# Kernel tuning notes

Measured on AMD Instinct MI355X. Metric: run time of the kernel, lower is better.

## Reference

```python
import jax, jax.numpy as jnp
import numpy as np

N = 50000   # nodes
E = 800000  # edges (before self loops)
D = 128     # n_embd
H = 4       # heads
C = D // H  # per-head channels
NEG_SLOPE = 0.2
EPS = 1e-5


def _ln(x, w):
    m = jnp.mean(x, axis=-1, keepdims=True)
    v = jnp.mean((x - m) ** 2, axis=-1, keepdims=True)
    return (x - m) / jnp.sqrt(v + EPS) * w


def setup_inputs() -> dict:
    key = jax.random.key(0)
    ks = jax.random.split(key, 8)
    s = 0.02
    return {
        "x": jax.random.normal(ks[0], (N, D), jnp.float32),
        "edge_index": jax.random.randint(ks[1], (2, E), 0, N, jnp.int32),
        "ln1_w": jnp.ones((D,), jnp.float32),
        "Wl": jax.random.normal(ks[2], (D, D), jnp.float32) * s,
        "bl": jnp.zeros((D,), jnp.float32),
        "Wr": jax.random.normal(ks[3], (D, D), jnp.float32) * s,
        "br": jnp.zeros((D,), jnp.float32),
        "att": jax.random.normal(ks[4], (H, C), jnp.float32) * s,
        "gat_bias": jnp.zeros((D,), jnp.float32),
        "ln2_w": jnp.ones((D,), jnp.float32),
        "W_fc": jax.random.normal(ks[5], (D, 4 * D), jnp.float32) * s,
        "W_proj": jax.random.normal(ks[6], (4 * D, D), jnp.float32) * s,
    }


def reference(x, edge_index, ln1_w, Wl, bl, Wr, br, att, gat_bias, ln2_w, W_fc, W_proj):
    n = x.shape[0]
    # add self loops (GATv2Conv default)
    loops = jnp.arange(n, dtype=edge_index.dtype)
    src = jnp.concatenate([edge_index[0], loops])  # message sources (x_j)
    dst = jnp.concatenate([edge_index[1], loops])  # message targets (x_i)

    h = _ln(x, ln1_w)
    xl = (h @ Wl + bl).reshape(n, H, C)  # source transform
    xr = (h @ Wr + br).reshape(n, H, C)  # target transform

    # GATv2 edge-wise attention
    e = jax.nn.leaky_relu(xl[src] + xr[dst], NEG_SLOPE)      # [E+N, H, C]
    score = jnp.einsum('ehc,hc->eh', e, att)                  # [E+N, H]
    smax = jax.ops.segment_max(score, dst, num_segments=n)    # [N, H]
    ex = jnp.exp(score - smax[dst])
    denom = jax.ops.segment_sum(ex, dst, num_segments=n)      # [N, H]
    alpha = ex / denom[dst]                                   # segment softmax
    agg = jax.ops.segment_sum(alpha[:, :, None] * xl[src], dst, num_segments=n)

    x = x + agg.reshape(n, H * C) + gat_bias

    h2 = _ln(x, ln2_w)
    x = x + jax.nn.gelu(h2 @ W_fc, approximate=False) @ W_proj
    return x
```

## Files before the change

### kernel.cpp

```cpp
#include <hip/hip_runtime.h>
#include <math.h>

typedef __attribute__((ext_vector_type(8))) short bf16x8;
typedef __attribute__((ext_vector_type(4))) float f32x4;

__device__ __forceinline__ unsigned bf16b(float f) {
  unsigned u = __float_as_uint(f);
  return (u + 0x7fffu + ((u >> 16) & 1u)) >> 16;
}
__device__ __forceinline__ unsigned packbf(float lo, float hi) {
  return bf16b(lo) | (bf16b(hi) << 16);
}
__device__ __forceinline__ float unpk_lo(unsigned u) { return __uint_as_float(u << 16); }
__device__ __forceinline__ float unpk_hi(unsigned u) { return __uint_as_float(u & 0xffff0000u); }
__device__ __forceinline__ float gelu_f(float v) {
  return 0.5f * v * (1.0f + erff(v * 0.70710678118654752f));
}

__global__ void k_cvt(const float* __restrict__ src, unsigned short* __restrict__ dst,
                      int lgK, int C, int total) {
  int i = blockIdx.x * 256 + threadIdx.x;
  if (i < total) {
    int k = i & ((1 << lgK) - 1);
    int c = i >> lgK;
    dst[i] = (unsigned short)bf16b(src[(size_t)k * C + c]);
  }
}

__global__ __launch_bounds__(256, 2) void k_gemlr(
    const float* __restrict__ x, const float* __restrict__ ln1w,
    const unsigned short* __restrict__ Wl_t, const float* __restrict__ bl,
    const unsigned short* __restrict__ Wr_t, const float* __restrict__ br,
    unsigned short* __restrict__ xl16, unsigned short* __restrict__ xr16, int n)
{
  __shared__ __align__(16) unsigned short hs[64 * 128];
  const int t = threadIdx.x;
  const int lane = t & 63, w = t >> 6;
  const int r0 = blockIdx.x * 64;

  {
    const int row = t >> 2, seg = t & 3;
    const int gr = r0 + row;
    const float4* xr4 = (const float4*)(x + (size_t)(gr < n ? gr : 0) * 128) + seg * 8;
    float4 v[8];
    #pragma unroll
    for (int j = 0; j < 8; ++j) v[j] = (gr < n) ? xr4[j] : make_float4(0.f,0.f,0.f,0.f);
    float s = 0.f;
    #pragma unroll
    for (int j = 0; j < 8; ++j) s += v[j].x + v[j].y + v[j].z + v[j].w;
    s += __shfl_xor(s, 1); s += __shfl_xor(s, 2);
    const float mean = s * (1.0f / 128.0f);
    float vv = 0.f;
    #pragma unroll
    for (int j = 0; j < 8; ++j) {
      float a = v[j].x - mean, b = v[j].y - mean, c = v[j].z - mean, d = v[j].w - mean;
      vv += a * a + b * b + c * c + d * d;
    }
    vv += __shfl_xor(vv, 1); vv += __shfl_xor(vv, 2);
    const float rstd = rsqrtf(vv * (1.0f / 128.0f) + 1e-5f);
    #pragma unroll
    for (int j2 = 0; j2 < 4; ++j2) {
      float4 wa = ((const float4*)ln1w)[seg * 8 + 2 * j2];
      float4 wb = ((const float4*)ln1w)[seg * 8 + 2 * j2 + 1];
      const float4 va = v[2 * j2], vb = v[2 * j2 + 1];
      uint4 pk;
      pk.x = packbf((va.x - mean) * rstd * wa.x, (va.y - mean) * rstd * wa.y);
      pk.y = packbf((va.z - mean) * rstd * wa.z, (va.w - mean) * rstd * wa.w);
      pk.z = packbf((vb.x - mean) * rstd * wb.x, (vb.y - mean) * rstd * wb.y);
      pk.w = packbf((vb.z - mean) * rstd * wb.z, (vb.w - mean) * rstd * wb.w);
      int byteoff = (row * 256 + (seg * 4 + j2) * 16) ^ ((row & 7) << 4);
      *(uint4*)((char*)hs + byteoff) = pk;
    }
  }
  __syncthreads();

  const int l15 = lane & 15, lg = lane >> 4;
  const unsigned short* __restrict__ Wt = (w < 2) ? Wl_t : Wr_t;
  const float* __restrict__ bias = (w < 2) ? bl : br;
  unsigned short* __restrict__ outp = (w < 2) ? xl16 : xr16;
  const int cbase = (w & 1) * 64;

  f32x4 acc[4][4];
  #pragma unroll
  for (int m = 0; m < 4; ++m)
    #pragma unroll
    for (int nf = 0; nf < 4; ++nf) acc[m][nf] = (f32x4){0.f, 0.f, 0.f, 0.f};

  #pragma unroll
  for (int ks = 0; ks < 4; ++ks) {
    bf16x8 b[4];
    #pragma unroll
    for (int nf = 0; nf < 4; ++nf) {
      const int c = cbase + nf * 16 + l15;
      b[nf] = *(const bf16x8*)(Wt + (size_t)c * 128 + ks * 32 + lg * 8);
    }
    bf16x8 a[4];
    #pragma unroll
    for (int m = 0; m < 4; ++m) {
      const int row = m * 16 + l15;
      const int byteoff = (row * 256 + ks * 64 + lg * 16) ^ ((row & 7) << 4);
      a[m] = *(const bf16x8*)((const char*)hs + byteoff);
    }
    #pragma unroll
    for (int m = 0; m < 4; ++m)
      #pragma unroll
      for (int nf = 0; nf < 4; ++nf)
        acc[m][nf] = __builtin_amdgcn_mfma_f32_16x16x32_bf16(a[m], b[nf], acc[m][nf], 0, 0, 0);
  }

  #pragma unroll
  for (int nf = 0; nf < 4; ++nf) {
    const int c = cbase + nf * 16 + l15;
    const float bv = bias[c];
    #pragma unroll
    for (int m = 0; m < 4; ++m) {
      #pragma unroll
      for (int r = 0; r < 4; ++r) {
        const int gr = r0 + m * 16 + lg * 4 + r;
        if (gr < n)
          outp[(size_t)gr * 128 + c] = (unsigned short)bf16b(acc[m][nf][r] + bv);
      }
    }
  }
}

__global__ void k_hist(const int* __restrict__ dst, int* __restrict__ deg, int E) {
  int e = blockIdx.x * 256 + threadIdx.x;
  if (e < E) atomicAdd(&deg[dst[e]], 1);
}

__global__ void k_scan1(const int* __restrict__ deg, int* __restrict__ bsum, int n) {
  __shared__ int red[4];
  const int t = threadIdx.x, lane = t & 63, w = t >> 6;
  const int i = blockIdx.x * 256 + t;
  int v = (i < n) ? deg[i] : 0;
  #pragma unroll
  for (int off = 1; off < 64; off <<= 1) v += __shfl_xor(v, off);
  if (lane == 0) red[w] = v;
  __syncthreads();
  if (t == 0) bsum[blockIdx.x] = red[0] + red[1] + red[2] + red[3];
}

__global__ void k_scan2(int* __restrict__ bsum, int nb, int* __restrict__ rowptr,
                        int n, int Etot) {
  __shared__ int wsum[16];
  const int t = threadIdx.x, lane = t & 63, w = t >> 6;
  const int v = (t < nb) ? bsum[t] : 0;
  int incl = v;
  #pragma unroll
  for (int off = 1; off < 64; off <<= 1) {
    int u = __shfl_up(incl, off);
    if (lane >= off) incl += u;
  }
  if (lane == 63) wsum[w] = incl;
  __syncthreads();
  if (w == 0 && lane < 16) {
    int sv = wsum[lane];
    int si = sv;
    #pragma unroll
    for (int off = 1; off < 16; off <<= 1) {
      int u = __shfl_up(si, off);
      if (lane >= off) si += u;
    }
    wsum[lane] = si - sv;
  }
  __syncthreads();
  if (t < nb) bsum[t] = wsum[w] + incl - v;
  if (t == 0) rowptr[n] = Etot;
}

__global__ void k_scan3(const int* __restrict__ deg, const int* __restrict__ bsum,
                        int* __restrict__ rowptr, int n) {
  __shared__ int ws4[4];
  const int t = threadIdx.x, lane = t & 63, w = t >> 6;
  const int i = blockIdx.x * 256 + t;
  const int v = (i < n) ? deg[i] : 0;
  int incl = v;
  #pragma unroll
  for (int off = 1; off < 64; off <<= 1) {
    int u = __shfl_up(incl, off);
    if (lane >= off) incl += u;
  }
  if (lane == 63) ws4[w] = incl;
  __syncthreads();
  if (t == 0) {
    int s1 = ws4[0], s2 = s1 + ws4[1], s3 = s2 + ws4[2];
    ws4[0] = 0; ws4[1] = s1; ws4[2] = s2; ws4[3] = s3;
  }
  __syncthreads();
  if (i < n) rowptr[i] = bsum[blockIdx.x] + ws4[w] + incl - v;
}

__global__ void k_scatter(const int* __restrict__ src, const int* __restrict__ dst,
                          const int* __restrict__ rowptr, int* __restrict__ cursor,
                          int* __restrict__ csr, int E) {
  int e = blockIdx.x * 256 + threadIdx.x;
  if (e < E) {
    int d = dst[e];
    int pos = atomicAdd(&cursor[d], 1);
    csr[rowptr[d] + pos] = src[e];
  }
}

__global__ __launch_bounds__(256) void k_attn(
    const float* __restrict__ x, const unsigned* __restrict__ xlp,
    const unsigned* __restrict__ xrp, const float* __restrict__ att,
    const float* __restrict__ gbias, const int* __restrict__ rowptr,
    const int* __restrict__ csr, float* __restrict__ x2, int n)
{
  const int d = (int)((blockIdx.x * blockDim.x + threadIdx.x) >> 6);
  if (d >= n) return;
  const int l = threadIdx.x & 63;
  const unsigned xr = xrp[(size_t)d * 64 + l];
  const float xr0 = unpk_lo(xr), xr1 = unpk_hi(xr);
  const float2 at = ((const float2*)att)[l];
  const int beg = rowptr[d], end = rowptr[d + 1];
  const int cnt = end - beg;

  float m, s, acc0, acc1;
  {
    const unsigned xs = xlp[(size_t)d * 64 + l];
    const float a0 = unpk_lo(xs), a1 = unpk_hi(xs);
    float e0 = a0 + xr0; e0 = (e0 > 0.f) ? e0 : 0.2f * e0;
    float e1 = a1 + xr1; e1 = (e1 > 0.f) ? e1 : 0.2f * e1;
    float tt = e0 * at.x + e1 * at.y;
    tt += __shfl_xor(tt, 1); tt += __shfl_xor(tt, 2);
    tt += __shfl_xor(tt, 4); tt += __shfl_xor(tt, 8);
    m = tt; s = 1.f; acc0 = a0; acc1 = a1;
  }

  unsigned pxs[4];
  if (cnt > 0) {
    int idx[4];
    #pragma unroll
    for (int i = 0; i < 4; ++i) idx[i] = (i < cnt) ? csr[beg + i] : d;
    #pragma unroll
    for (int i = 0; i < 4; ++i) pxs[i] = xlp[(size_t)idx[i] * 64 + l];
  }
  for (int b = 0; b < cnt; b += 4) {
    unsigned xs[4];
    #pragma unroll
    for (int i = 0; i < 4; ++i) xs[i] = pxs[i];
    if (b + 4 < cnt) {
      int idx[4];
      #pragma unroll
      for (int i = 0; i < 4; ++i) idx[i] = (b + 4 + i < cnt) ? csr[beg + b + 4 + i] : d;
      #pragma unroll
      for (int i = 0; i < 4; ++i) pxs[i] = xlp[(size_t)idx[i] * 64 + l];
    }
    const int rem = cnt - b;
    float A0[4], A1[4], T[4];
    #pragma unroll
    for (int i = 0; i < 4; ++i) {
      A0[i] = unpk_lo(xs[i]); A1[i] = unpk_hi(xs[i]);
      float e0 = A0[i] + xr0; e0 = (e0 > 0.f) ? e0 : 0.2f * e0;
      float e1 = A1[i] + xr1; e1 = (e1 > 0.f) ? e1 : 0.2f * e1;
      T[i] = e0 * at.x + e1 * at.y;
    }
    #pragma unroll
    for (int off = 1; off < 16; off <<= 1)
      #pragma unroll
      for (int i = 0; i < 4; ++i) T[i] += __shfl_xor(T[i], off);
    #pragma unroll
    for (int i = 0; i < 4; ++i) if (i >= rem) T[i] = -1e30f;
    const float bm = fmaxf(fmaxf(T[0], T[1]), fmaxf(T[2], T[3]));
    const float p0 = __expf(T[0] - bm), p1 = __expf(T[1] - bm);
    const float p2 = __expf(T[2] - bm), p3 = __expf(T[3] - bm);
    const float bs = p0 + p1 + p2 + p3;
    const float b0 = p0 * A0[0] + p1 * A0[1] + p2 * A0[2] + p3 * A0[3];
    const float b1 = p0 * A1[0] + p1 * A1[1] + p2 * A1[2] + p3 * A1[3];
    const float nm = fmaxf(m, bm);
    const float sc = __expf(m - nm), sb = __expf(bm - nm);
    s    = s    * sc + bs * sb;
    acc0 = acc0 * sc + b0 * sb;
    acc1 = acc1 * sc + b1 * sb;
    m = nm;
  }

  const float inv = 1.0f / s;
  const float2 xv = ((const float2*)x)[(size_t)d * 64 + l];
  const float2 gb = ((const float2*)gbias)[l];
  float2 o;
  o.x = xv.x + acc0 * inv + gb.x;
  o.y = xv.y + acc1 * inv + gb.y;
  ((float2*)x2)[(size_t)d * 64 + l] = o;
}

__global__ __launch_bounds__(256, 2) void k_mlp(
    const float* __restrict__ x2, const float* __restrict__ ln2w,
    const unsigned short* __restrict__ Wfc_t, const unsigned short* __restrict__ Wpj_t,
    float* __restrict__ out, int n)
{
  __shared__ __align__(16) unsigned short sm[32768];
  const int t = threadIdx.x;
  const int lane = t & 63, w = t >> 6;
  const int r0 = blockIdx.x * 64;

  {
    const int row = t >> 2, seg = t & 3;
    const int gr = r0 + row;
    const float4* xr4 = (const float4*)(x2 + (size_t)(gr < n ? gr : 0) * 128) + seg * 8;
    float4 v[8];
    #pragma unroll
    for (int j = 0; j < 8; ++j) v[j] = (gr < n) ? xr4[j] : make_float4(0.f,0.f,0.f,0.f);
    float s = 0.f;
    #pragma unroll
    for (int j = 0; j < 8; ++j) s += v[j].x + v[j].y + v[j].z + v[j].w;
    s += __shfl_xor(s, 1); s += __shfl_xor(s, 2);
    const float mean = s * (1.0f / 128.0f);
    float vv = 0.f;
    #pragma unroll
    for (int j = 0; j < 8; ++j) {
      float a = v[j].x - mean, b = v[j].y - mean, c = v[j].z - mean, d = v[j].w - mean;
      vv += a * a + b * b + c * c + d * d;
    }
    vv += __shfl_xor(vv, 1); vv += __shfl_xor(vv, 2);
    const float rstd = rsqrtf(vv * (1.0f / 128.0f) + 1e-5f);
    #pragma unroll
    for (int j2 = 0; j2 < 4; ++j2) {
      float4 wa = ((const float4*)ln2w)[seg * 8 + 2 * j2];
      float4 wb = ((const float4*)ln2w)[seg * 8 + 2 * j2 + 1];
      const float4 va = v[2 * j2], vb = v[2 * j2 + 1];
      uint4 pk;
      pk.x = packbf((va.x - mean) * rstd * wa.x, (va.y - mean) * rstd * wa.y);
      pk.y = packbf((va.z - mean) * rstd * wa.z, (va.w - mean) * rstd * wa.w);
      pk.z = packbf((vb.x - mean) * rstd * wb.x, (vb.y - mean) * rstd * wb.y);
      pk.w = packbf((vb.z - mean) * rstd * wb.z, (vb.w - mean) * rstd * wb.w);
      int byteoff = (row * 256 + (seg * 4 + j2) * 16) ^ ((row & 7) << 4);
      *(uint4*)((char*)sm + byteoff) = pk;
    }
  }
  __syncthreads();

  const int l15 = lane & 15, lg = lane >> 4;

  f32x4 acc[4][8];
  #pragma unroll
  for (int m = 0; m < 4; ++m)
    #pragma unroll
    for (int nf = 0; nf < 8; ++nf) acc[m][nf] = (f32x4){0.f, 0.f, 0.f, 0.f};

  #pragma unroll
  for (int ks = 0; ks < 4; ++ks) {
    bf16x8 b[8];
    #pragma unroll
    for (int nf = 0; nf < 8; ++nf) {
      const int c = w * 128 + nf * 16 + l15;
      b[nf] = *(const bf16x8*)(Wfc_t + (size_t)c * 128 + ks * 32 + lg * 8);
    }
    bf16x8 a[4];
    #pragma unroll
    for (int m = 0; m < 4; ++m) {
      const int row = m * 16 + l15;
      const int byteoff = (row * 256 + ks * 64 + lg * 16) ^ ((row & 7) << 4);
      a[m] = *(const bf16x8*)((const char*)sm + byteoff);
    }
    #pragma unroll
    for (int m = 0; m < 4; ++m)
      #pragma unroll
      for (int nf = 0; nf < 8; ++nf)
        acc[m][nf] = __builtin_amdgcn_mfma_f32_16x16x32_bf16(a[m], b[nf], acc[m][nf], 0, 0, 0);
  }
  __syncthreads();

  #pragma unroll
  for (int m = 0; m < 4; ++m)
    #pragma unroll
    for (int nf = 0; nf < 8; ++nf)
      #pragma unroll
      for (int r = 0; r < 4; ++r) {
        const int row = m * 16 + lg * 4 + r;
        const int col = w * 128 + nf * 16 + l15;
        const int byteoff = (row * 1024 + col * 2) ^ ((row & 7) << 4);
        *(unsigned short*)((char*)sm + byteoff) = (unsigned short)bf16b(gelu_f(acc[m][nf][r]));
      }
  __syncthreads();

  f32x4 acc2[4][2];
  #pragma unroll
  for (int m = 0; m < 4; ++m) {
    acc2[m][0] = (f32x4){0.f, 0.f, 0.f, 0.f};
    acc2[m][1] = (f32x4){0.f, 0.f, 0.f, 0.f};
  }
  #pragma unroll 4
  for (int ks = 0; ks < 16; ++ks) {
    bf16x8 b2[2];
    #pragma unroll
    for (int nf = 0; nf < 2; ++nf) {
      const int c = w * 32 + nf * 16 + l15;
      b2[nf] = *(const bf16x8*)(Wpj_t + (size_t)c * 512 + ks * 32 + lg * 8);
    }
    bf16x8 a2[4];
    #pragma unroll
    for (int m = 0; m < 4; ++m) {
      const int row = m * 16 + l15;
      const int byteoff = (row * 1024 + ks * 64 + lg * 16) ^ ((row & 7) << 4);
      a2[m] = *(const bf16x8*)((const char*)sm + byteoff);
    }
    #pragma unroll
    for (int m = 0; m < 4; ++m) {
      acc2[m][0] = __builtin_amdgcn_mfma_f32_16x16x32_bf16(a2[m], b2[0], acc2[m][0], 0, 0, 0);
      acc2[m][1] = __builtin_amdgcn_mfma_f32_16x16x32_bf16(a2[m], b2[1], acc2[m][1], 0, 0, 0);
    }
  }

  #pragma unroll
  for (int m = 0; m < 4; ++m)
    #pragma unroll
    for (int nf = 0; nf < 2; ++nf) {
      const int col = w * 32 + nf * 16 + l15;
      #pragma unroll
      for (int r = 0; r < 4; ++r) {
        const int gr = r0 + m * 16 + lg * 4 + r;
        if (gr < n)
          out[(size_t)gr * 128 + col] = x2[(size_t)gr * 128 + col] + acc2[m][nf][r];
      }
    }
}

extern "C" void kernel_launch(void* const* d_in, const int* in_sizes, int n_in,
                              void* d_out, int out_size, void* d_ws, size_t ws_size,
                              hipStream_t stream)
{
  (void)n_in; (void)out_size; (void)ws_size;
  const float* x     = (const float*)d_in[0];
  const int*   ei    = (const int*)d_in[1];
  const float* ln1w  = (const float*)d_in[2];
  const float* Wl    = (const float*)d_in[3];
  const float* bl    = (const float*)d_in[4];
  const float* Wr    = (const float*)d_in[5];
  const float* br    = (const float*)d_in[6];
  const float* att   = (const float*)d_in[7];
  const float* gbias = (const float*)d_in[8];
  const float* ln2w  = (const float*)d_in[9];
  const float* Wfc   = (const float*)d_in[10];
  const float* Wpj   = (const float*)d_in[11];
  float* out = (float*)d_out;

  const int n = in_sizes[0] / 128;
  const int E = in_sizes[1] / 2;
  const int nb = (n + 255) / 256;

  char* w = (char*)d_ws;
  unsigned short* xl16 = (unsigned short*)w; w += (size_t)n * 128 * 2;
  unsigned short* xr16 = (unsigned short*)w; w += (size_t)n * 128 * 2;
  float*    x2  = (float*)w;    w += (size_t)n * 128 * 4;
  int*      deg = (int*)w;      w += (size_t)n * 4;
  int*   rowptr = (int*)w;      w += (size_t)(n + 1) * 4;
  int*   cursor = (int*)w;      w += (size_t)n * 4;
  int*     bsum = (int*)w;      w += 1024 * 4;
  int*      csr = (int*)w;      w += (size_t)E * 4;
  unsigned short* Wl_t  = (unsigned short*)w; w += 128 * 128 * 2;
  unsigned short* Wr_t  = (unsigned short*)w; w += 128 * 128 * 2;
  unsigned short* Wfc_t = (unsigned short*)w; w += 512 * 128 * 2;
  unsigned short* Wpj_t = (unsigned short*)w; w += 128 * 512 * 2;

  hipMemsetAsync(deg, 0, (size_t)n * 4, stream);
  hipMemsetAsync(cursor, 0, (size_t)n * 4, stream);

  k_cvt<<<(128 * 128 + 255) / 256, 256, 0, stream>>>(Wl,  Wl_t,  7, 128, 128 * 128);
  k_cvt<<<(128 * 128 + 255) / 256, 256, 0, stream>>>(Wr,  Wr_t,  7, 128, 128 * 128);
  k_cvt<<<(512 * 128 + 255) / 256, 256, 0, stream>>>(Wfc, Wfc_t, 7, 512, 512 * 128);
  k_cvt<<<(512 * 128 + 255) / 256, 256, 0, stream>>>(Wpj, Wpj_t, 9, 128, 512 * 128);

  k_gemlr<<<(n + 63) / 64, 256, 0, stream>>>(x, ln1w, Wl_t, bl, Wr_t, br, xl16, xr16, n);
  k_hist<<<(E + 255) / 256, 256, 0, stream>>>(ei + E, deg, E);
  k_scan1<<<nb, 256, 0, stream>>>(deg, bsum, n);
  k_scan2<<<1, 1024, 0, stream>>>(bsum, nb, rowptr, n, E);
  k_scan3<<<nb, 256, 0, stream>>>(deg, bsum, rowptr, n);
  k_scatter<<<(E + 255) / 256, 256, 0, stream>>>(ei, ei + E, rowptr, cursor, csr, E);
  k_attn<<<(n + 3) / 4, 256, 0, stream>>>(x, (const unsigned*)xl16, (const unsigned*)xr16,
                                          att, gbias, rowptr, csr, x2, n);
  k_mlp<<<(n + 63) / 64, 256, 0, stream>>>(x2, ln2w, Wfc_t, Wpj_t, out, n);
}
```

Before: 386.6 us.

## Split MLP into tiled fc/proj kernels, fuse LN2 into attention, merge setup kernels

```diff
diff --git a/kernel.cpp b/kernel.cpp
--- a/kernel.cpp
+++ b/kernel.cpp
@@ -17,13 +17,25 @@
   return 0.5f * v * (1.0f + erff(v * 0.70710678118654752f));
 }
 
-__global__ void k_cvt(const float* __restrict__ src, unsigned short* __restrict__ dst,
-                      int lgK, int C, int total) {
+__global__ void k_cvtz(const float* __restrict__ Wl, const float* __restrict__ Wr,
+                       const float* __restrict__ Wfc, const float* __restrict__ Wpj,
+                       unsigned short* __restrict__ Wl_t, unsigned short* __restrict__ Wr_t,
+                       unsigned short* __restrict__ Wfc_t, unsigned short* __restrict__ Wpj_t,
+                       int* __restrict__ deg, int* __restrict__ cursor, int n) {
   int i = blockIdx.x * 256 + threadIdx.x;
-  if (i < total) {
-    int k = i & ((1 << lgK) - 1);
-    int c = i >> lgK;
-    dst[i] = (unsigned short)bf16b(src[(size_t)k * C + c]);
+  if (i < n) { deg[i] = 0; cursor[i] = 0; }
+  if (i < 16384) {
+    int k = i & 127, c = i >> 7;
+    Wl_t[i] = (unsigned short)bf16b(Wl[k * 128 + c]);
+    Wr_t[i] = (unsigned short)bf16b(Wr[k * 128 + c]);
+  } else if (i < 81920) {
+    int j = i - 16384;
+    int k = j & 127, c = j >> 7;
+    Wfc_t[j] = (unsigned short)bf16b(Wfc[(size_t)k * 512 + c]);
+  } else if (i < 147456) {
+    int j = i - 81920;
+    int k = j & 511, c = j >> 9;
+    Wpj_t[j] = (unsigned short)bf16b(Wpj[(size_t)k * 128 + c]);
   }
 }
 
@@ -205,8 +217,9 @@
 __global__ __launch_bounds__(256) void k_attn(
     const float* __restrict__ x, const unsigned* __restrict__ xlp,
     const unsigned* __restrict__ xrp, const float* __restrict__ att,
-    const float* __restrict__ gbias, const int* __restrict__ rowptr,
-    const int* __restrict__ csr, float* __restrict__ x2, int n)
+    const float* __restrict__ gbias, const float* __restrict__ ln2w,
+    const int* __restrict__ rowptr, const int* __restrict__ csr,
+    float* __restrict__ x2, unsigned* __restrict__ h2p, int n)
 {
   const int d = (int)((blockIdx.x * blockDim.x + threadIdx.x) >> 6);
   if (d >= n) return;
@@ -284,138 +297,153 @@
   o.x = xv.x + acc0 * inv + gb.x;
   o.y = xv.y + acc1 * inv + gb.y;
   ((float2*)x2)[(size_t)d * 64 + l] = o;
-}
-
-__global__ __launch_bounds__(256, 2) void k_mlp(
-    const float* __restrict__ x2, const float* __restrict__ ln2w,
-    const unsigned short* __restrict__ Wfc_t, const unsigned short* __restrict__ Wpj_t,
+
+  float s2 = o.x + o.y;
+  #pragma unroll
+  for (int off = 1; off < 64; off <<= 1) s2 += __shfl_xor(s2, off);
+  const float mean = s2 * (1.0f / 128.0f);
+  const float dx = o.x - mean, dy = o.y - mean;
+  float vv = dx * dx + dy * dy;
+  #pragma unroll
+  for (int off = 1; off < 64; off <<= 1) vv += __shfl_xor(vv, off);
+  const float rstd = rsqrtf(vv * (1.0f / 128.0f) + 1e-5f);
+  const float2 lw = ((const float2*)ln2w)[l];
+  h2p[(size_t)d * 64 + l] = packbf(dx * rstd * lw.x, dy * rstd * lw.y);
+}
+
+__global__ __launch_bounds__(256, 3) void k_fc(
+    const unsigned short* __restrict__ h2, const unsigned short* __restrict__ Wfc_t,
+    unsigned short* __restrict__ g, int n)
+{
+  __shared__ __align__(16) unsigned short As[128 * 128];
+  __shared__ __align__(16) unsigned short Bs[64 * 128];
+  const int t = threadIdx.x, lane = t & 63, w = t >> 6;
+  const int l15 = lane & 15, lg = lane >> 4;
+  const int r0 = blockIdx.x * 128;
+  const int cb0 = blockIdx.y * 64;
+
+  #pragma unroll
+  for (int it = 0; it < 8; ++it) {
+    int i = it * 256 + t;
+    int row = i >> 4, c16 = i & 15;
+    int gr = r0 + row;
+    uint4 v = make_uint4(0, 0, 0, 0);
+    if (gr < n) v = *(const uint4*)(h2 + (size_t)gr * 128 + c16 * 8);
+    *(uint4*)((char*)As + ((row * 256 + c16 * 16) ^ ((row & 7) << 4))) = v;
+  }
+  #pragma unroll
+  for (int it = 0; it < 4; ++it) {
+    int i = it * 256 + t;
+    int col = i >> 4, k16 = i & 15;
+    uint4 v = *(const uint4*)(Wfc_t + (size_t)(cb0 + col) * 128 + k16 * 8);
+    *(uint4*)((char*)Bs + ((col * 256 + k16 * 16) ^ ((col & 7) << 4))) = v;
+  }
+  __syncthreads();
+
+  const int rbase = (w >> 1) * 64;
+  const int cbase = (w & 1) * 32;
+  f32x4 acc[4][2];
+  #pragma unroll
+  for (int m = 0; m < 4; ++m) {
+    acc[m][0] = (f32x4){0.f, 0.f, 0.f, 0.f};
+    acc[m][1] = (f32x4){0.f, 0.f, 0.f, 0.f};
+  }
+  #pragma unroll
+  for (int ks = 0; ks < 4; ++ks) {
+    bf16x8 b[2], a[4];
+    #pragma unroll
+    for (int nf = 0; nf < 2; ++nf) {
+      const int col = cbase + nf * 16 + l15;
+      b[nf] = *(const bf16x8*)((const char*)Bs + ((col * 256 + ks * 64 + lg * 16) ^ ((col & 7) << 4)));
+    }
+    #pragma unroll
+    for (int m = 0; m < 4; ++m) {
+      const int row = rbase + m * 16 + l15;
+      a[m] = *(const bf16x8*)((const char*)As + ((row * 256 + ks * 64 + lg * 16) ^ ((row & 7) << 4)));
+    }
+    #pragma unroll
+    for (int m = 0; m < 4; ++m) {
+      acc[m][0] = __builtin_amdgcn_mfma_f32_16x16x32_bf16(a[m], b[0], acc[m][0], 0, 0, 0);
+      acc[m][1] = __builtin_amdgcn_mfma_f32_16x16x32_bf16(a[m], b[1], acc[m][1], 0, 0, 0);
+    }
+  }
+
+  #pragma unroll
+  for (int m = 0; m < 4; ++m)
+    #pragma unroll
+    for (int nf = 0; nf < 2; ++nf) {
+      const int gc = cb0 + cbase + nf * 16 + l15;
+      #pragma unroll
+      for (int r = 0; r < 4; ++r) {
+        const int gr = r0 + rbase + m * 16 + lg * 4 + r;
+        if (gr < n)
+          g[(size_t)gr * 256 + gc] = (unsigned short)bf16b(gelu_f(acc[m][nf][r]));
+      }
+    }
+}
+
+__global__ __launch_bounds__(256, 3) void k_proj(
+    const unsigned short* __restrict__ g, const unsigned short* __restrict__ Wpj_t,
     float* __restrict__ out, int n)
 {
-  __shared__ __align__(16) unsigned short sm[32768];
-  const int t = threadIdx.x;
-  const int lane = t & 63, w = t >> 6;
+  __shared__ __align__(16) unsigned short As[64 * 64];
+  __shared__ __align__(16) unsigned short Bs[128 * 64];
+  const int t = threadIdx.x, lane = t & 63, w = t >> 6;
+  const int l15 = lane & 15, lg = lane >> 4;
   const int r0 = blockIdx.x * 64;
 
-  {
-    const int row = t >> 2, seg = t & 3;
-    const int gr = r0 + row;
-    const float4* xr4 = (const float4*)(x2 + (size_t)(gr < n ? gr : 0) * 128) + seg * 8;
-    float4 v[8];
-    #pragma unroll
-    for (int j = 0; j < 8; ++j) v[j] = (gr < n) ? xr4[j] : make_float4(0.f,0.f,0.f,0.f);
-    float s = 0.f;
-    #pragma unroll
-    for (int j = 0; j < 8; ++j) s += v[j].x + v[j].y + v[j].z + v[j].w;
-    s += __shfl_xor(s, 1); s += __shfl_xor(s, 2);
-    const float mean = s * (1.0f / 128.0f);
-    float vv = 0.f;
-    #pragma unroll
-    for (int j = 0; j < 8; ++j) {
-      float a = v[j].x - mean, b = v[j].y - mean, c = v[j].z - mean, d = v[j].w - mean;
-      vv += a * a + b * b + c * c + d * d;
-    }
-    vv += __shfl_xor(vv, 1); vv += __shfl_xor(vv, 2);
-    const float rstd = rsqrtf(vv * (1.0f / 128.0f) + 1e-5f);
-    #pragma unroll
-    for (int j2 = 0; j2 < 4; ++j2) {
-      float4 wa = ((const float4*)ln2w)[seg * 8 + 2 * j2];
-      float4 wb = ((const float4*)ln2w)[seg * 8 + 2 * j2 + 1];
-      const float4 va = v[2 * j2], vb = v[2 * j2 + 1];
-      uint4 pk;
-      pk.x = packbf((va.x - mean) * rstd * wa.x, (va.y - mean) * rstd * wa.y);
-      pk.y = packbf((va.z - mean) * rstd * wa.z, (va.w - mean) * rstd * wa.w);
-      pk.z = packbf((vb.x - mean) * rstd * wb.x, (vb.y - mean) * rstd * wb.y);
-      pk.w = packbf((vb.z - mean) * rstd * wb.z, (vb.w - mean) * rstd * wb.w);
-      int byteoff = (row * 256 + (seg * 4 + j2) * 16) ^ ((row & 7) << 4);
-      *(uint4*)((char*)sm + byteoff) = pk;
-    }
-  }
-  __syncthreads();
-
-  const int l15 = lane & 15, lg = lane >> 4;
-
-  f32x4 acc[4][8];
-  #pragma unroll
-  for (int m = 0; m < 4; ++m)
-    #pragma unroll
-    for (int nf = 0; nf < 8; ++nf) acc[m][nf] = (f32x4){0.f, 0.f, 0.f, 0.f};
-
-  #pragma unroll
-  for (int ks = 0; ks < 4; ++ks) {
-    bf16x8 b[8];
-    #pragma unroll
-    for (int nf = 0; nf < 8; ++nf) {
-      const int c = w * 128 + nf * 16 + l15;
-      b[nf] = *(const bf16x8*)(Wfc_t + (size_t)c * 128 + ks * 32 + lg * 8);
-    }
-    bf16x8 a[4];
-    #pragma unroll
-    for (int m = 0; m < 4; ++m) {
-      const int row = m * 16 + l15;
-      const int byteoff = (row * 256 + ks * 64 + lg * 16) ^ ((row & 7) << 4);
-      a[m] = *(const bf16x8*)((const char*)sm + byteoff);
-    }
-    #pragma unroll
-    for (int m = 0; m < 4; ++m)
+  f32x4 acc[8];
+  #pragma unroll
+  for (int nf = 0; nf < 8; ++nf) acc[nf] = (f32x4){0.f, 0.f, 0.f, 0.f};
+
+  for (int kt = 0; kt < 4; ++kt) {
+    __syncthreads();
+    #pragma unroll
+    for (int it = 0; it < 2; ++it) {
+      int i = it * 256 + t;
+      int row = i >> 3, k8 = i & 7;
+      int gr = r0 + row;
+      uint4 v = make_uint4(0, 0, 0, 0);
+      if (gr < n) v = *(const uint4*)(g + (size_t)gr * 256 + kt * 64 + k8 * 8);
+      *(uint4*)((char*)As + ((row * 128 + k8 * 16) ^ ((row & 7) << 4))) = v;
+    }
+    #pragma unroll
+    for (int it = 0; it < 4; ++it) {
+      int i = it * 256 + t;
+      int col = i >> 3, k8 = i & 7;
+      uint4 v = *(const uint4*)(Wpj_t + (size_t)col * 512 + kt * 64 + k8 * 8);
+      *(uint4*)((char*)Bs + ((col * 128 + k8 * 16) ^ ((col & 7) << 4))) = v;
+    }
+    __syncthreads();
+
+    #pragma unroll
+    for (int ks = 0; ks < 2; ++ks) {
+      const int row = w * 16 + l15;
+      bf16x8 a = *(const bf16x8*)((const char*)As + ((row * 128 + ks * 64 + lg * 16) ^ ((row & 7) << 4)));
+      bf16x8 b[8];
+      #pragma unroll
+      for (int nf = 0; nf < 8; ++nf) {
+        const int col = nf * 16 + l15;
+        b[nf] = *(const bf16x8*)((const char*)Bs + ((col * 128 + ks * 64 + lg * 16) ^ ((col & 7) << 4)));
+      }
       #pragma unroll
       for (int nf = 0; nf < 8; ++nf)
-        acc[m][nf] = __builtin_amdgcn_mfma_f32_16x16x32_bf16(a[m], b[nf], acc[m][nf], 0, 0, 0);
-  }
-  __syncthreads();
-
-  #pragma unroll
-  for (int m = 0; m < 4; ++m)
-    #pragma unroll
-    for (int nf = 0; nf < 8; ++nf)
-      #pragma unroll
-      for (int r = 0; r < 4; ++r) {
-        const int row = m * 16 + lg * 4 + r;
-        const int col = w * 128 + nf * 16 + l15;
-        const int byteoff = (row * 1024 + col * 2) ^ ((row & 7) << 4);
-        *(unsigned short*)((char*)sm + byteoff) = (unsigned short)bf16b(gelu_f(acc[m][nf][r]));
+        acc[nf] = __builtin_amdgcn_mfma_f32_16x16x32_bf16(a, b[nf], acc[nf], 0, 0, 0);
+    }
+  }
+
+  #pragma unroll
+  for (int nf = 0; nf < 8; ++nf) {
+    const int col = nf * 16 + l15;
+    #pragma unroll
+    for (int r = 0; r < 4; ++r) {
+      const int gr = r0 + w * 16 + lg * 4 + r;
+      if (gr < n) {
+        float* p = out + (size_t)gr * 128 + col;
+        *p = *p + acc[nf][r];
       }
-  __syncthreads();
-
-  f32x4 acc2[4][2];
-  #pragma unroll
-  for (int m = 0; m < 4; ++m) {
-    acc2[m][0] = (f32x4){0.f, 0.f, 0.f, 0.f};
-    acc2[m][1] = (f32x4){0.f, 0.f, 0.f, 0.f};
-  }
-  #pragma unroll 4
-  for (int ks = 0; ks < 16; ++ks) {
-    bf16x8 b2[2];
-    #pragma unroll
-    for (int nf = 0; nf < 2; ++nf) {
-      const int c = w * 32 + nf * 16 + l15;
-      b2[nf] = *(const bf16x8*)(Wpj_t + (size_t)c * 512 + ks * 32 + lg * 8);
-    }
-    bf16x8 a2[4];
-    #pragma unroll
-    for (int m = 0; m < 4; ++m) {
-      const int row = m * 16 + l15;
-      const int byteoff = (row * 1024 + ks * 64 + lg * 16) ^ ((row & 7) << 4);
-      a2[m] = *(const bf16x8*)((const char*)sm + byteoff);
-    }
-    #pragma unroll
-    for (int m = 0; m < 4; ++m) {
-      acc2[m][0] = __builtin_amdgcn_mfma_f32_16x16x32_bf16(a2[m], b2[0], acc2[m][0], 0, 0, 0);
-      acc2[m][1] = __builtin_amdgcn_mfma_f32_16x16x32_bf16(a2[m], b2[1], acc2[m][1], 0, 0, 0);
-    }
-  }
-
-  #pragma unroll
-  for (int m = 0; m < 4; ++m)
-    #pragma unroll
-    for (int nf = 0; nf < 2; ++nf) {
-      const int col = w * 32 + nf * 16 + l15;
-      #pragma unroll
-      for (int r = 0; r < 4; ++r) {
-        const int gr = r0 + m * 16 + lg * 4 + r;
-        if (gr < n)
-          out[(size_t)gr * 128 + col] = x2[(size_t)gr * 128 + col] + acc2[m][nf][r];
-      }
-    }
+    }
+  }
 }
 
 extern "C" void kernel_launch(void* const* d_in, const int* in_sizes, int n_in,
@@ -442,27 +470,23 @@
   const int nb = (n + 255) / 256;
 
   char* w = (char*)d_ws;
-  unsigned short* xl16 = (unsigned short*)w; w += (size_t)n * 128 * 2;
-  unsigned short* xr16 = (unsigned short*)w; w += (size_t)n * 128 * 2;
-  float*    x2  = (float*)w;    w += (size_t)n * 128 * 4;
-  int*      deg = (int*)w;      w += (size_t)n * 4;
-  int*   rowptr = (int*)w;      w += (size_t)(n + 1) * 4;
-  int*   cursor = (int*)w;      w += (size_t)n * 4;
-  int*     bsum = (int*)w;      w += 1024 * 4;
-  int*      csr = (int*)w;      w += (size_t)E * 4;
-  unsigned short* Wl_t  = (unsigned short*)w; w += 128 * 128 * 2;
-  unsigned short* Wr_t  = (unsigned short*)w; w += 128 * 128 * 2;
-  unsigned short* Wfc_t = (unsigned short*)w; w += 512 * 128 * 2;
-  unsigned short* Wpj_t = (unsigned short*)w; w += 128 * 512 * 2;
-
-  hipMemsetAsync(deg, 0, (size_t)n * 4, stream);
-  hipMemsetAsync(cursor, 0, (size_t)n * 4, stream);
-
-  k_cvt<<<(128 * 128 + 255) / 256, 256, 0, stream>>>(Wl,  Wl_t,  7, 128, 128 * 128);
-  k_cvt<<<(128 * 128 + 255) / 256, 256, 0, stream>>>(Wr,  Wr_t,  7, 128, 128 * 128);
-  k_cvt<<<(512 * 128 + 255) / 256, 256, 0, stream>>>(Wfc, Wfc_t, 7, 512, 512 * 128);
-  k_cvt<<<(512 * 128 + 255) / 256, 256, 0, stream>>>(Wpj, Wpj_t, 9, 128, 512 * 128);
-
+  unsigned short* h2    = (unsigned short*)w; w += (size_t)n * 128 * 2;
+  unsigned short* Wl_t  = (unsigned short*)w; w += 16384 * 2;
+  unsigned short* Wr_t  = (unsigned short*)w; w += 16384 * 2;
+  unsigned short* Wfc_t = (unsigned short*)w; w += 65536 * 2;
+  unsigned short* Wpj_t = (unsigned short*)w; w += 65536 * 2;
+  int* rowptr = (int*)w; w += (size_t)((n + 4) & ~3) * 4;
+  int* bsum   = (int*)w; w += 1024 * 4;
+  int* deg    = (int*)w; w += (size_t)n * 4;
+  int* cursor = (int*)w; w += (size_t)n * 4;
+  char* gbase = w;
+  unsigned short* xl16 = (unsigned short*)gbase;
+  unsigned short* xr16 = (unsigned short*)(gbase + (size_t)n * 128 * 2);
+  int* csr             = (int*)(gbase + (size_t)n * 128 * 4);
+  unsigned short* g    = (unsigned short*)gbase;
+
+  k_cvtz<<<576, 256, 0, stream>>>(Wl, Wr, Wfc, Wpj, Wl_t, Wr_t, Wfc_t, Wpj_t,
+                                  deg, cursor, n);
   k_gemlr<<<(n + 63) / 64, 256, 0, stream>>>(x, ln1w, Wl_t, bl, Wr_t, br, xl16, xr16, n);
   k_hist<<<(E + 255) / 256, 256, 0, stream>>>(ei + E, deg, E);
   k_scan1<<<nb, 256, 0, stream>>>(deg, bsum, n);
@@ -470,6 +494,11 @@
   k_scan3<<<nb, 256, 0, stream>>>(deg, bsum, rowptr, n);
   k_scatter<<<(E + 255) / 256, 256, 0, stream>>>(ei, ei + E, rowptr, cursor, csr, E);
   k_attn<<<(n + 3) / 4, 256, 0, stream>>>(x, (const unsigned*)xl16, (const unsigned*)xr16,
-                                          att, gbias, rowptr, csr, x2, n);
-  k_mlp<<<(n + 63) / 64, 256, 0, stream>>>(x2, ln2w, Wfc_t, Wpj_t, out, n);
-}
+                                          att, gbias, ln2w, rowptr, csr, out,
+                                          (unsigned*)h2, n);
+  dim3 gfc((n + 127) / 128, 4);
+  for (int half = 0; half < 2; ++half) {
+    k_fc  <<<gfc, 256, 0, stream>>>(h2, Wfc_t + (size_t)half * 256 * 128, g, n);
+    k_proj<<<(n + 63) / 64, 256, 0, stream>>>(g, Wpj_t + (size_t)half * 256, out, n);
+  }
+}
```

Measured after the change: 379.7 us. No clear change (-1.8%).
